# Kernel tuning notes

Hardware: AMD Instinct MI355X
Metric: run time of the kernel (lower is better)

## Reference

```python
import jax, jax.numpy as jnp
import numpy as np

B, H, N, D = 2, 16, 2048, 64

def setup_inputs() -> dict:
    key = jax.random.key(0)
    ks = jax.random.split(key, 5)
    q = jax.random.normal(ks[0], (B, H, N, D), dtype=jnp.float32)
    k = jax.random.normal(ks[1], (B, H, N, D), dtype=jnp.float32)
    v = jax.random.normal(ks[2], (B, H, N, D), dtype=jnp.float32)
    # 1x1 Conv2d(heads, heads, bias=False) == HxH linear mixing over the head dim
    W_pre = jax.random.normal(ks[3], (H, H), dtype=jnp.float32) * (1.0 / jnp.sqrt(H))
    W_post = jax.random.normal(ks[4], (H, H), dtype=jnp.float32) * (1.0 / jnp.sqrt(H))
    return {"q": q, "k": k, "v": v, "W_pre": W_pre, "W_post": W_post}

def reference(q, k, v, W_pre, W_post):
    heads = q.shape[1]
    d_head = q.shape[-1]
    # original: scale = (1/sqrt(heads)) / sqrt(d_head)
    scale = 1.0 / (jnp.sqrt(jnp.float32(heads)) * jnp.sqrt(jnp.float32(d_head)))
    # pre-softmax talking heads applied to BOTH q and k (head-mixing linear)
    q = jnp.einsum('ef,bfnd->bend', W_pre, q)
    k = jnp.einsum('ef,bfnd->bend', W_pre, k)
    attn_weights = jnp.einsum('bhid,bhjd->bhij', q, k) * scale  # [B,H,N,N]
    i = q.shape[-2]
    j = k.shape[-2]
    causal_mask = jnp.triu(jnp.ones((i, j), dtype=bool), k=1)
    attn_weights = jnp.where(causal_mask, -jnp.inf, attn_weights)
    # softmax computed in float32 (dtype=torch.float32 in attn_fn)
    attn_probs = jax.nn.softmax(attn_weights.astype(jnp.float32), axis=-1)
    # dropout p=0.0 -> identity
    attn_probs = jnp.einsum('ef,bfij->beij', W_post, attn_probs)
    attn_output = jnp.einsum('bhij,bhjd->bhid', attn_probs, v)
    return attn_output
```

## Files before the change

kernel.cpp:

```cpp
#include <hip/hip_runtime.h>
#include <math.h>

typedef _Float16 Hh;
typedef __attribute__((ext_vector_type(8))) _Float16 half8;
typedef __attribute__((ext_vector_type(4))) _Float16 half4;
typedef __attribute__((ext_vector_type(4))) float float4v;

#define B_ 2
#define H_ 16
#define N_ 2048
#define D_ 64
#define ND_ (N_*D_)
#define C1 0.04508422f

#define BAR() asm volatile("s_waitcnt lgkmcnt(0)\n\ts_barrier" ::: "memory")

#define EB_JS 644
#define EB_IS 20
#define PM_ES 1156
#define PM_IS 36

__global__ void prep_kernel(const float* __restrict__ q,
    const float* __restrict__ k, const float* __restrict__ v,
    const float* __restrict__ Wpre,
    Hh* __restrict__ qb, Hh* __restrict__ kb, Hh* __restrict__ vt2,
    float4* __restrict__ out4, float4* __restrict__ lacc4)
{
    int tid = threadIdx.x;
    int bid = blockIdx.x;
    if (bid < 512) {
        __shared__ float wsh[256];
        wsh[tid] = Wpre[tid];
        __syncthreads();
        int tensor = bid >> 8;
        int g = ((bid & 255) << 8) | tid;
        int b = g >> 15;
        int r = g & 32767;
        const float4* src = (const float4*)(tensor ? k : q);
        Hh* dst = tensor ? kb : qb;
        float4 x[16];
        #pragma unroll
        for (int f=0; f<16; f++) x[f] = src[(size_t)(b*16+f)*32768 + r];
        #pragma unroll
        for (int e=0; e<16; e++) {
            float4 a = make_float4(0.f,0.f,0.f,0.f);
            #pragma unroll
            for (int f=0; f<16; f++) {
                float wv = wsh[e*16+f];
                a.x += wv*x[f].x; a.y += wv*x[f].y; a.z += wv*x[f].z; a.w += wv*x[f].w;
            }
            half4 hv; hv[0]=(Hh)a.x; hv[1]=(Hh)a.y; hv[2]=(Hh)a.z; hv[3]=(Hh)a.w;
            *(half4*)(dst + (size_t)(b*16+e)*ND_ + (size_t)r*4) = hv;
        }
    } else if (bid < 768) {
        __shared__ Hh tile[64*48];
        int tb = bid - 512;
        int be = tb >> 3;
        int jtg = tb & 7;
        const float4* v4 = (const float4*)v;
        for (int u=0; u<8; u++) {
            int jt = jtg*8 + u;
            #pragma unroll
            for (int p=0; p<2; p++) {
                int j = p*16 + (tid>>4);
                int d4 = tid & 15;
                float4 val = v4[(size_t)be*32768 + (size_t)(jt*32+j)*16 + d4];
                tile[(d4*4+0)*48 + j] = (Hh)val.x;
                tile[(d4*4+1)*48 + j] = (Hh)val.y;
                tile[(d4*4+2)*48 + j] = (Hh)val.z;
                tile[(d4*4+3)*48 + j] = (Hh)val.w;
            }
            BAR();
            {
                int d = tid >> 2;
                int jc = (tid & 3) * 8;
                half8 o;
                #pragma unroll
                for (int z=0; z<8; z++) o[z] = tile[d*48 + jc + z];
                *(half8*)(vt2 + ((size_t)(be*64) + jt)*2048 + (size_t)tid*8) = o;
            }
            BAR();
        }
    } else {
        int zid = (bid - 768) * 256 + tid;
        float4 zz = make_float4(0.f,0.f,0.f,0.f);
        #pragma unroll
        for (int u=0; u<4; u++) out4[(size_t)u*262144 + zid] = zz;
        if (zid < 16384) lacc4[zid] = zz;
    }
}

__global__ __launch_bounds__(1024)
__attribute__((amdgpu_waves_per_eu(4,4)))
void denom_kernel(const Hh* __restrict__ qb,
    const Hh* __restrict__ kb, float* __restrict__ lacc_g)
{
    int bid = blockIdx.x;
    int s = bid & 7;
    int idx = bid >> 3;
    int b = idx & 1;
    int pr = idx >> 1;
    int tid = threadIdx.x;
    int lane = tid & 63, w = tid >> 6;
    int qd = lane >> 4, c = lane & 15;

    const Hh* qh = qb + (size_t)(b*16 + w)*ND_;
    const Hh* kh = kb + (size_t)(b*16 + w)*ND_;

    for (int hf = 0; hf < 2; hf++) {
        int it = hf ? (31 - pr) : pr;
        int i0 = it * 64;

        half8 aq[4][2];
        #pragma unroll
        for (int ig=0; ig<4; ig++) {
            const Hh* qr = qh + (size_t)(i0 + ig*16 + c)*64 + qd*8;
            aq[ig][0] = *(const half8*)qr;
            aq[ig][1] = *(const half8*)(qr+32);
        }
        float lacc[4][4];
        #pragma unroll
        for (int ig=0; ig<4; ig++)
            #pragma unroll
            for (int r=0; r<4; r++) lacc[ig][r] = 0.f;

        int jtmax = 2*it + 1;
        for (int jt = s; jt <= jtmax; jt += 8) {
            int j0 = jt*32;
            #pragma unroll
            for (int jh=0; jh<2; jh++) {
                const Hh* kr = kh + (size_t)(j0 + jh*16 + c)*64 + qd*8;
                half8 b0 = *(const half8*)kr;
                half8 b1 = *(const half8*)(kr+32);
                int j = j0 + jh*16 + c;
                #pragma unroll
                for (int ig=0; ig<4; ig++) {
                    float4v sv = {0.f,0.f,0.f,0.f};
                    sv = __builtin_amdgcn_mfma_f32_16x16x32_f16(aq[ig][0], b0, sv, 0,0,0);
                    sv = __builtin_amdgcn_mfma_f32_16x16x32_f16(aq[ig][1], b1, sv, 0,0,0);
                    #pragma unroll
                    for (int r=0; r<4; r++) {
                        int i = i0 + ig*16 + qd*4 + r;
                        float ev = (j <= i) ? __builtin_amdgcn_exp2f(sv[r]*C1) : 0.f;
                        lacc[ig][r] += ev;
                    }
                }
            }
        }
        #pragma unroll
        for (int ig=0; ig<4; ig++) {
            #pragma unroll
            for (int r=0; r<4; r++) {
                float vs = lacc[ig][r];
                vs += __shfl_xor(vs, 1);
                vs += __shfl_xor(vs, 2);
                vs += __shfl_xor(vs, 4);
                vs += __shfl_xor(vs, 8);
                if (c == 0)
                    unsafeAtomicAdd(&lacc_g[(size_t)(b*16+w)*N_ + i0 + ig*16 + qd*4 + r], vs);
            }
        }
    }
}

__global__ __launch_bounds__(1024)
__attribute__((amdgpu_waves_per_eu(4,4)))
void attend_kernel(const Hh* __restrict__ qb,
    const Hh* __restrict__ kb, const Hh* __restrict__ vt2,
    const float* __restrict__ lacc_g, const float* __restrict__ Wpost,
    float* __restrict__ out)
{
    __shared__ Hh Ebuf[32*EB_JS];
    __shared__ Hh Pm[16*PM_ES];

    int bid = blockIdx.x;
    int s = (bid & 7) >> 1;
    int b = bid & 1;
    int pr = bid >> 3;

    int tid = threadIdx.x;
    int lane = tid & 63, w = tid >> 6;
    int qd = lane >> 4, c = lane & 15;

    int jh2 = w & 1, ib = 4*(w >> 1);
    half4 wf;
    #pragma unroll
    for (int z=0; z<4; z++) wf[z] = (Hh)Wpost[c*16 + qd*4 + z];

    for (int hf = 0; hf < 2; hf++) {
        int it = hf ? (63 - pr) : pr;
        if (s > it) continue;
        int i0 = it * 32;

        half8 aq[2][2];
        float lgr[2][4];
        #pragma unroll
        for (int ig=0; ig<2; ig++) {
            const Hh* qr = qb + (size_t)((b*16+w)*N_ + i0 + ig*16 + c)*64 + qd*8;
            aq[ig][0] = *(const half8*)qr;
            aq[ig][1] = *(const half8*)(qr+32);
            #pragma unroll
            for (int r=0; r<4; r++)
                lgr[ig][r] = __builtin_amdgcn_logf(
                    lacc_g[(size_t)(b*16+w)*N_ + i0 + ig*16 + qd*4 + r]);
        }

        float4v acc[2][4];
        #pragma unroll
        for (int ig=0; ig<2; ig++) for (int nc=0; nc<4; nc++)
            acc[ig][nc] = (float4v){0.f,0.f,0.f,0.f};

        auto loadK = [&](int jt, half8 (&kk)[2][2]) {
            #pragma unroll
            for (int jh=0; jh<2; jh++) {
                const Hh* kr = kb + (size_t)((b*16+w)*N_ + jt*32 + jh*16 + c)*64 + qd*8;
                kk[jh][0] = *(const half8*)kr;
                kk[jh][1] = *(const half8*)(kr+32);
            }
        };
        auto loadV = [&](int jt, half8 (&vv)[4]) {
            #pragma unroll
            for (int nc=0; nc<4; nc++)
                vv[nc] = *(const half8*)(vt2 +
                    (size_t)((b*16+w)*64 + jt)*2048 + (nc*16+c)*32 + qd*8);
        };

        auto scores = [&](int jt, half8 (&kk)[2][2]) {
            #pragma unroll
            for (int jh=0; jh<2; jh++) {
                int j = jt*32 + jh*16 + c;
                #pragma unroll
                for (int ig=0; ig<2; ig++) {
                    float4v sv = {0.f,0.f,0.f,0.f};
                    sv = __builtin_amdgcn_mfma_f32_16x16x32_f16(aq[ig][0], kk[jh][0], sv, 0,0,0);
                    sv = __builtin_amdgcn_mfma_f32_16x16x32_f16(aq[ig][1], kk[jh][1], sv, 0,0,0);
                    #pragma unroll
                    for (int r=0; r<4; r++) {
                        int i = i0 + ig*16 + qd*4 + r;
                        float ev = (j <= i) ?
                            __builtin_amdgcn_exp2f(sv[r]*C1 - lgr[ig][r]) : 0.f;
                        Ebuf[(size_t)(jh*16+c)*EB_JS + (ig*16+qd*4+r)*EB_IS + w] = (Hh)ev;
                    }
                }
            }
        };

        half8 kk[2][2], vv[4];
        loadK(s, kk);
        loadV(s, vv);
        scores(s, kk);
        BAR();

        for (int jt = s; jt <= it; jt += 4) {
            bool more = (jt + 4 <= it);
            half8 kn[2][2], vn[4];
            if (more) { loadK(jt + 4, kn); loadV(jt + 4, vn); }
            #pragma unroll
            for (int ii=0; ii<4; ii++) {
                int i = ib + ii;
                half4 ef = *(const half4*)&Ebuf[(jh2*16+c)*EB_JS + i*EB_IS + qd*4];
                float4v cc = {0.f,0.f,0.f,0.f};
                cc = __builtin_amdgcn_mfma_f32_16x16x16f16(ef, wf, cc, 0,0,0);
                half4 hv;
                #pragma unroll
                for (int r=0; r<4; r++) hv[r] = (Hh)cc[r];
                *(half4*)&Pm[c*PM_ES + i*PM_IS + jh2*16 + qd*4] = hv;
            }
            BAR();
            #pragma unroll
            for (int nc=0; nc<4; nc++) {
                #pragma unroll
                for (int ig=0; ig<2; ig++) {
                    half8 pa = *(const half8*)&Pm[w*PM_ES + (ig*16+c)*PM_IS + qd*8];
                    acc[ig][nc] = __builtin_amdgcn_mfma_f32_16x16x32_f16(pa, vv[nc], acc[ig][nc], 0,0,0);
                }
            }
            if (more) {
                scores(jt + 4, kn);
                #pragma unroll
                for (int nc=0; nc<4; nc++) vv[nc] = vn[nc];
            }
            BAR();
        }

        #pragma unroll
        for (int ig=0; ig<2; ig++) {
            #pragma unroll
            for (int nc0=0; nc0<4; nc0++) {
                int nc = (nc0 + s) & 3;
                #pragma unroll
                for (int r=0; r<4; r++)
                    unsafeAtomicAdd(&out[(size_t)((b*16+w)*N_ + i0 + ig*16 + qd*4 + r)*64 + nc*16 + c],
                                    acc[ig][nc][r]);
            }
        }
    }
}

extern "C" void kernel_launch(void* const* d_in, const int* in_sizes, int n_in,
                              void* d_out, int out_size, void* d_ws, size_t ws_size,
                              hipStream_t stream) {
    const float* q     = (const float*)d_in[0];
    const float* k     = (const float*)d_in[1];
    const float* v     = (const float*)d_in[2];
    const float* Wpre  = (const float*)d_in[3];
    const float* Wpost = (const float*)d_in[4];
    float* out = (float*)d_out;

    size_t tsz = (size_t)B_*H_*N_*D_;
    Hh* qb = (Hh*)d_ws;
    Hh* kb = qb + tsz;
    Hh* vt2 = kb + tsz;
    float* lacc = (float*)(vt2 + tsz);

    prep_kernel<<<1792, 256, 0, stream>>>(q, k, v, Wpre, qb, kb, vt2,
                                          (float4*)out, (float4*)lacc);
    denom_kernel<<<256, 1024, 0, stream>>>(qb, kb, lacc);
    attend_kernel<<<256, 1024, 0, stream>>>(qb, kb, vt2, lacc, Wpost, out);
}
```

Before: 229.3 us.

## Fuse softmax denominator pass into attend kernel with inter-block counter sync

Removes the separate denom kernel and computes the per-row exp sums inside the attend kernel. The four blocks sharing a query tile each add their partial sums atomically, bump a per-tile counter, and spin until all four have arrived before reading the log-denominator. This saves a kernel launch and the second full read of Q/K, but assumes all cooperating blocks are co-resident, which risks deadlock, and adds spin-wait and fence overhead. The workspace zeroing is extended to clear the counters.

```diff
diff --git a/kernel.cpp b/kernel.cpp
--- a/kernel.cpp
+++ b/kernel.cpp
@@ -86,80 +86,7 @@
         float4 zz = make_float4(0.f,0.f,0.f,0.f);
         #pragma unroll
         for (int u=0; u<4; u++) out4[(size_t)u*262144 + zid] = zz;
-        if (zid < 16384) lacc4[zid] = zz;
-    }
-}
-
-__global__ __launch_bounds__(1024)
-__attribute__((amdgpu_waves_per_eu(4,4)))
-void denom_kernel(const Hh* __restrict__ qb,
-    const Hh* __restrict__ kb, float* __restrict__ lacc_g)
-{
-    int bid = blockIdx.x;
-    int s = bid & 7;
-    int idx = bid >> 3;
-    int b = idx & 1;
-    int pr = idx >> 1;
-    int tid = threadIdx.x;
-    int lane = tid & 63, w = tid >> 6;
-    int qd = lane >> 4, c = lane & 15;
-
-    const Hh* qh = qb + (size_t)(b*16 + w)*ND_;
-    const Hh* kh = kb + (size_t)(b*16 + w)*ND_;
-
-    for (int hf = 0; hf < 2; hf++) {
-        int it = hf ? (31 - pr) : pr;
-        int i0 = it * 64;
-
-        half8 aq[4][2];
-        #pragma unroll
-        for (int ig=0; ig<4; ig++) {
-            const Hh* qr = qh + (size_t)(i0 + ig*16 + c)*64 + qd*8;
-            aq[ig][0] = *(const half8*)qr;
-            aq[ig][1] = *(const half8*)(qr+32);
-        }
-        float lacc[4][4];
-        #pragma unroll
-        for (int ig=0; ig<4; ig++)
-            #pragma unroll
-            for (int r=0; r<4; r++) lacc[ig][r] = 0.f;
-
-        int jtmax = 2*it + 1;
-        for (int jt = s; jt <= jtmax; jt += 8) {
-            int j0 = jt*32;
-            #pragma unroll
-            for (int jh=0; jh<2; jh++) {
-                const Hh* kr = kh + (size_t)(j0 + jh*16 + c)*64 + qd*8;
-                half8 b0 = *(const half8*)kr;
-                half8 b1 = *(const half8*)(kr+32);
-                int j = j0 + jh*16 + c;
-                #pragma unroll
-                for (int ig=0; ig<4; ig++) {
-                    float4v sv = {0.f,0.f,0.f,0.f};
-                    sv = __builtin_amdgcn_mfma_f32_16x16x32_f16(aq[ig][0], b0, sv, 0,0,0);
-                    sv = __builtin_amdgcn_mfma_f32_16x16x32_f16(aq[ig][1], b1, sv, 0,0,0);
-                    #pragma unroll
-                    for (int r=0; r<4; r++) {
-                        int i = i0 + ig*16 + qd*4 + r;
-                        float ev = (j <= i) ? __builtin_amdgcn_exp2f(sv[r]*C1) : 0.f;
-                        lacc[ig][r] += ev;
-                    }
-                }
-            }
-        }
-        #pragma unroll
-        for (int ig=0; ig<4; ig++) {
-            #pragma unroll
-            for (int r=0; r<4; r++) {
-                float vs = lacc[ig][r];
-                vs += __shfl_xor(vs, 1);
-                vs += __shfl_xor(vs, 2);
-                vs += __shfl_xor(vs, 4);
-                vs += __shfl_xor(vs, 8);
-                if (c == 0)
-                    unsafeAtomicAdd(&lacc_g[(size_t)(b*16+w)*N_ + i0 + ig*16 + qd*4 + r], vs);
-            }
-        }
+        if (zid < 16416) lacc4[zid] = zz;
     }
 }
 
@@ -167,12 +94,14 @@
 __attribute__((amdgpu_waves_per_eu(4,4)))
 void attend_kernel(const Hh* __restrict__ qb,
     const Hh* __restrict__ kb, const Hh* __restrict__ vt2,
-    const float* __restrict__ lacc_g, const float* __restrict__ Wpost,
+    float* __restrict__ lacc_g, const float* __restrict__ Wpost,
     float* __restrict__ out)
 {
     __shared__ Hh Ebuf[32*EB_JS];
     __shared__ Hh Pm[16*PM_ES];
 
+    int* cnt = (int*)(lacc_g + 65536);
+
     int bid = blockIdx.x;
     int s = (bid & 7) >> 1;
     int b = bid & 1;
@@ -189,26 +118,17 @@
 
     for (int hf = 0; hf < 2; hf++) {
         int it = hf ? (63 - pr) : pr;
-        if (s > it) continue;
         int i0 = it * 32;
+        int ci = b*64 + it;
+        bool active = (s <= it);
 
         half8 aq[2][2];
-        float lgr[2][4];
         #pragma unroll
         for (int ig=0; ig<2; ig++) {
             const Hh* qr = qb + (size_t)((b*16+w)*N_ + i0 + ig*16 + c)*64 + qd*8;
             aq[ig][0] = *(const half8*)qr;
             aq[ig][1] = *(const half8*)(qr+32);
-            #pragma unroll
-            for (int r=0; r<4; r++)
-                lgr[ig][r] = __builtin_amdgcn_logf(
-                    lacc_g[(size_t)(b*16+w)*N_ + i0 + ig*16 + qd*4 + r]);
-        }
-
-        float4v acc[2][4];
-        #pragma unroll
-        for (int ig=0; ig<2; ig++) for (int nc=0; nc<4; nc++)
-            acc[ig][nc] = (float4v){0.f,0.f,0.f,0.f};
+        }
 
         auto loadK = [&](int jt, half8 (&kk)[2][2]) {
             #pragma unroll
@@ -218,6 +138,73 @@
                 kk[jh][1] = *(const half8*)(kr+32);
             }
         };
+
+        if (active) {
+            float ls[2][4];
+            #pragma unroll
+            for (int ig=0; ig<2; ig++)
+                #pragma unroll
+                for (int r=0; r<4; r++) ls[ig][r] = 0.f;
+
+            for (int jt = s; jt <= it; jt += 4) {
+                half8 kk[2][2];
+                loadK(jt, kk);
+                #pragma unroll
+                for (int jh=0; jh<2; jh++) {
+                    int j = jt*32 + jh*16 + c;
+                    #pragma unroll
+                    for (int ig=0; ig<2; ig++) {
+                        float4v sv = {0.f,0.f,0.f,0.f};
+                        sv = __builtin_amdgcn_mfma_f32_16x16x32_f16(aq[ig][0], kk[jh][0], sv, 0,0,0);
+                        sv = __builtin_amdgcn_mfma_f32_16x16x32_f16(aq[ig][1], kk[jh][1], sv, 0,0,0);
+                        #pragma unroll
+                        for (int r=0; r<4; r++) {
+                            int i = i0 + ig*16 + qd*4 + r;
+                            float ev = (j <= i) ? __builtin_amdgcn_exp2f(sv[r]*C1) : 0.f;
+                            ls[ig][r] += ev;
+                        }
+                    }
+                }
+            }
+            #pragma unroll
+            for (int ig=0; ig<2; ig++) {
+                #pragma unroll
+                for (int r=0; r<4; r++) {
+                    float vs = ls[ig][r];
+                    vs += __shfl_xor(vs, 1);
+                    vs += __shfl_xor(vs, 2);
+                    vs += __shfl_xor(vs, 4);
+                    vs += __shfl_xor(vs, 8);
+                    if (c == 0)
+                        unsafeAtomicAdd(&lacc_g[(size_t)(b*16+w)*N_ + i0 + ig*16 + qd*4 + r], vs);
+                }
+            }
+        }
+        __threadfence();
+        __syncthreads();
+        if (tid == 0)
+            __hip_atomic_fetch_add(&cnt[ci], 1, __ATOMIC_RELEASE, __HIP_MEMORY_SCOPE_AGENT);
+        if (!active) continue;
+        if (tid == 0) {
+            while (__hip_atomic_load(&cnt[ci], __ATOMIC_ACQUIRE, __HIP_MEMORY_SCOPE_AGENT) < 4)
+                __builtin_amdgcn_s_sleep(8);
+        }
+        __syncthreads();
+        __threadfence();
+
+        float lgr[2][4];
+        #pragma unroll
+        for (int ig=0; ig<2; ig++)
+            #pragma unroll
+            for (int r=0; r<4; r++)
+                lgr[ig][r] = __builtin_amdgcn_logf(
+                    lacc_g[(size_t)(b*16+w)*N_ + i0 + ig*16 + qd*4 + r]);
+
+        float4v acc[2][4];
+        #pragma unroll
+        for (int ig=0; ig<2; ig++) for (int nc=0; nc<4; nc++)
+            acc[ig][nc] = (float4v){0.f,0.f,0.f,0.f};
+
         auto loadV = [&](int jt, half8 (&vv)[4]) {
             #pragma unroll
             for (int nc=0; nc<4; nc++)
@@ -315,6 +302,5 @@
 
     prep_kernel<<<1792, 256, 0, stream>>>(q, k, v, Wpre, qb, kb, vt2,
                                           (float4*)out, (float4*)lacc);
-    denom_kernel<<<256, 1024, 0, stream>>>(qb, kb, lacc);
     attend_kernel<<<256, 1024, 0, stream>>>(qb, kb, vt2, lacc, Wpost, out);
 }
```

Result: slower. 654.3 us (+185.3%).
